# Kernel tuning notes

Hardware: AMD Instinct MI355X
Metric: run time of the kernel (lower is better)

The kernel has to match this reference:

```python
import jax, jax.numpy as jnp
import numpy as np

N = 50000       # nodes
E = 800000      # edges (avg degree 16)
NFEAT = 256
NHID = 32
NHEADS = 4
ALPHA = 0.2     # leaky relu slope


def setup_inputs() -> dict:
    key = jax.random.key(0)
    ks = jax.random.split(key, 7)
    x = jax.random.normal(ks[0], (N, NFEAT), dtype=jnp.float32)
    src = jax.random.randint(ks[1], (E,), 0, N, dtype=jnp.int32)
    dst = jax.random.randint(ks[2], (E,), 0, N, dtype=jnp.int32)
    Ws = jax.random.normal(ks[3], (NHEADS, NFEAT, NHID), dtype=jnp.float32) * 0.05
    As = jax.random.normal(ks[4], (NHEADS, 2 * NHID), dtype=jnp.float32) * 0.05
    Wo = jax.random.normal(ks[5], (NHID * NHEADS, NHID), dtype=jnp.float32) * 0.05
    Ao = jax.random.normal(ks[6], (2 * NHID,), dtype=jnp.float32) * 0.05
    return {"x": x, "src": src, "dst": dst, "Ws": Ws, "As": As, "Wo": Wo, "Ao": Ao}


def _gat_layer(h, src, dst, W, a, concat):
    # h: [N, F_in] -> project
    h = h @ W                          # [N, d]
    d = W.shape[1]
    hs = h[src]                        # [E, d] gather source feats
    hd = h[dst]                        # [E, d] gather neighbor feats
    # a . concat([hs, hd]) == hs @ a[:d] + hd @ a[d:]
    e = hs @ a[:d] + hd @ a[d:]        # [E]
    e = jnp.where(e > 0, e, ALPHA * e)  # leaky relu
    # segment softmax keyed on src
    m = jax.ops.segment_max(e, src, num_segments=N)    # [N]
    ex = jnp.exp(e - m[src])
    denom = jax.ops.segment_sum(ex, src, num_segments=N)  # [N]
    att = ex / denom[src]              # [E]
    # weighted neighbor aggregation (scatter-sum on src)
    h_prime = jax.ops.segment_sum(att[:, None] * hd, src, num_segments=N)  # [N, d]
    return jax.nn.elu(h_prime) if concat else h_prime


def reference(x, src, dst, Ws, As, Wo, Ao):
    heads = [_gat_layer(x, src, dst, Ws[i], As[i], concat=True) for i in range(NHEADS)]
    h = jnp.concatenate(heads, axis=1)                 # [N, nhid*nheads]
    out = jax.nn.elu(_gat_layer(h, src, dst, Wo, Ao, concat=False))  # [N, nhid]
    return out
```

## Files before the change

### kernel.cpp

```cpp
#include <hip/hip_runtime.h>
#include <hip/hip_fp16.h>
#include <math.h>

#define N_NODES 50000
#define N_EDGES 800000
#define NFEAT 256
#define NHID 32
#define NHEADS 4
#define ALPHA 0.2f
#define ELLCAP 64
#define ELLSH 6

typedef _Float16 half8_t __attribute__((ext_vector_type(8)));
typedef float f32x4 __attribute__((ext_vector_type(4)));

__device__ __forceinline__ float elu_f(float x) {
    return x > 0.0f ? x : (__expf(x) - 1.0f);
}

__device__ __forceinline__ float wexp(float x) {
    float l = x > 0.0f ? x : ALPHA * x;
    return __expf(l);
}

__device__ __forceinline__ float h2f_bits(unsigned wd, int sh) {
    ushort b = (ushort)(wd >> sh);
    return __half2float(*(__half*)&b);
}

__global__ void k_prep(const float* __restrict__ Ws, const float* __restrict__ Wo,
                       ushort* __restrict__ Wt1, ushort* __restrict__ Wt2) {
    int idx = blockIdx.x * 256 + threadIdx.x;
    if (idx < 128 * 256) {
        int c = idx >> 8;
        int k = idx & 255;
        __half hv = __float2half(Ws[(c >> 5) * (NFEAT * NHID) + k * NHID + (c & 31)]);
        Wt1[idx] = *(ushort*)&hv;
    } else if (idx < 128 * 256 + 32 * 128) {
        int j = idx - 128 * 256;
        int c = j >> 7;
        int k = j & 127;
        __half hv = __float2half(Wo[k * NHID + c]);
        Wt2[j] = *(ushort*)&hv;
    }
}

template <int K, int NTILES, bool AHALF, int NH>
__global__ __launch_bounds__(256) void k_gemm_mfma(const void* __restrict__ Ain,
                                                   const ushort* __restrict__ Wt,
                                                   const float* __restrict__ attn,
                                                   __half* __restrict__ C,
                                                   float* __restrict__ So,
                                                   float* __restrict__ Si,
                                                   int nrows) {
    constexpr int N = NTILES * 16;
    constexpr int BK = 32;
    constexpr int LDB = 40;

    __shared__ __align__(16) ushort Bs[N * LDB];

    int tid = threadIdx.x;
    int w = tid >> 6;
    int lane = tid & 63;
    int c = lane & 15;
    int quad = lane >> 4;
    int row0 = blockIdx.x * 64 + w * 16;
    int gm = row0 + c;
    if (gm >= nrows) gm = nrows - 1;

    f32x4 acc[NTILES];
#pragma unroll
    for (int nt = 0; nt < NTILES; nt++)
#pragma unroll
        for (int i = 0; i < 4; i++) acc[nt][i] = 0.0f;

    float a_so[NTILES], a_si[NTILES];
#pragma unroll
    for (int nt = 0; nt < NTILES; nt++) {
        int h = nt >> 1;
        a_so[nt] = attn[h * 64 + (nt & 1) * 16 + c];
        a_si[nt] = attn[h * 64 + 32 + (nt & 1) * 16 + c];
    }

    for (int k0 = 0; k0 < K; k0 += BK) {
        if (tid < N * 2) {
            int r = tid >> 1;
            int part = tid & 1;
            const uint4* gp = (const uint4*)(Wt + (size_t)r * K + k0 + part * 16);
            uint4 v0 = gp[0];
            uint4 v1 = gp[1];
            uint4* lp = (uint4*)&Bs[r * LDB + part * 16];
            lp[0] = v0;
            lp[1] = v1;
        }
        __syncthreads();

        half8_t ahi, alo;
        if constexpr (AHALF) {
            ahi = *(const half8_t*)((const ushort*)Ain + (size_t)gm * K + k0 + quad * 8);
        } else {
            const float* ap = (const float*)Ain + (size_t)gm * K + k0 + quad * 8;
            float4 x0 = *(const float4*)ap;
            float4 x1 = *(const float4*)(ap + 4);
            float xa[8] = {x0.x, x0.y, x0.z, x0.w, x1.x, x1.y, x1.z, x1.w};
#pragma unroll
            for (int j = 0; j < 8; j++) {
                _Float16 h = (_Float16)xa[j];
                ahi[j] = h;
                alo[j] = (_Float16)(xa[j] - (float)h);
            }
        }
#pragma unroll
        for (int nt = 0; nt < NTILES; nt++) {
            half8_t b = *(const half8_t*)&Bs[(nt * 16 + c) * LDB + quad * 8];
            acc[nt] = __builtin_amdgcn_mfma_f32_16x16x32_f16(ahi, b, acc[nt], 0, 0, 0);
            if constexpr (!AHALF)
                acc[nt] = __builtin_amdgcn_mfma_f32_16x16x32_f16(alo, b, acc[nt], 0, 0, 0);
        }
        __syncthreads();
    }

#pragma unroll
    for (int reg = 0; reg < 4; reg++) {
        int ro = row0 + quad * 4 + reg;
        bool ok = ro < nrows;
        if (ok) {
#pragma unroll
            for (int nt = 0; nt < NTILES; nt++)
                C[(size_t)ro * N + nt * 16 + c] = __float2half(acc[nt][reg]);
        }
#pragma unroll
        for (int h = 0; h < NH; h++) {
            float so = acc[2 * h][reg] * a_so[2 * h] + acc[2 * h + 1][reg] * a_so[2 * h + 1];
            float si = acc[2 * h][reg] * a_si[2 * h] + acc[2 * h + 1][reg] * a_si[2 * h + 1];
            so += __shfl_xor(so, 1); si += __shfl_xor(si, 1);
            so += __shfl_xor(so, 2); si += __shfl_xor(si, 2);
            so += __shfl_xor(so, 4); si += __shfl_xor(si, 4);
            so += __shfl_xor(so, 8); si += __shfl_xor(si, 8);
            if (c == 0 && ok) {
                So[(size_t)ro * NH + h] = so;
                Si[(size_t)ro * NH + h] = si;
            }
        }
    }
}

__global__ void k_fill(const int* __restrict__ src, const int* __restrict__ dst,
                       const float* __restrict__ S1o, const float* __restrict__ S1i,
                       int* __restrict__ deg, uint4* __restrict__ ell16,
                       int* __restrict__ eslot) {
    int e = blockIdx.x * 256 + threadIdx.x;
    if (e >= N_EDGES) return;
    int s = src[e];
    int v = dst[e];
    int slot = atomicAdd(&deg[s], 1);
    eslot[e] = slot;
    if (slot >= ELLCAP) return;
    float4 so = *(const float4*)(S1o + 4 * (size_t)s);
    float4 si = *(const float4*)(S1i + 4 * (size_t)v);
    __half2 w01 = __floats2half2_rn(wexp(so.x + si.x), wexp(so.y + si.y));
    __half2 w23 = __floats2half2_rn(wexp(so.z + si.z), wexp(so.w + si.w));
    uint4 q;
    q.x = (unsigned)v;
    q.y = *(unsigned*)&w01;
    q.z = *(unsigned*)&w23;
    q.w = 0;
    ell16[((size_t)s << ELLSH) + slot] = q;
}

__global__ __launch_bounds__(256) void k_aggw4(const int* __restrict__ deg,
                                               const uint4* __restrict__ ell16,
                                               const __half* __restrict__ H1h,
                                               __half* __restrict__ Hch) {
    int node = blockIdx.x * 4 + (threadIdx.x >> 6);
    if (node >= N_NODES) return;
    int lane = threadIdx.x & 63;
    int ha = lane >> 4;
    int sel = ha & 2;
    int sh = (ha & 1) * 16;
    int dg = deg[node];
    if (dg > ELLCAP) dg = ELLCAP;
    const uint4* lp = ell16 + ((size_t)node << ELLSH);
    const unsigned* Hp = (const unsigned*)H1h;
    float a0 = 0.0f, a1 = 0.0f, d = 0.0f;
    int j = 0;
    for (; j + 3 < dg; j += 4) {
        uint4 q0 = lp[j];
        uint4 q1 = lp[j + 1];
        uint4 q2 = lp[j + 2];
        uint4 q3 = lp[j + 3];
        unsigned u0 = Hp[((size_t)q0.x << 6) + lane];
        unsigned u1 = Hp[((size_t)q1.x << 6) + lane];
        unsigned u2 = Hp[((size_t)q2.x << 6) + lane];
        unsigned u3 = Hp[((size_t)q3.x << 6) + lane];
        float w0 = h2f_bits(sel ? q0.z : q0.y, sh);
        float w1 = h2f_bits(sel ? q1.z : q1.y, sh);
        float w2 = h2f_bits(sel ? q2.z : q2.y, sh);
        float w3 = h2f_bits(sel ? q3.z : q3.y, sh);
        float2 h0 = __half22float2(*(__half2*)&u0);
        float2 h1 = __half22float2(*(__half2*)&u1);
        float2 h2 = __half22float2(*(__half2*)&u2);
        float2 h3 = __half22float2(*(__half2*)&u3);
        a0 += w0 * h0.x; a1 += w0 * h0.y; d += w0;
        a0 += w1 * h1.x; a1 += w1 * h1.y; d += w1;
        a0 += w2 * h2.x; a1 += w2 * h2.y; d += w2;
        a0 += w3 * h3.x; a1 += w3 * h3.y; d += w3;
    }
    for (; j < dg; j++) {
        uint4 q0 = lp[j];
        unsigned u0 = Hp[((size_t)q0.x << 6) + lane];
        float w0 = h2f_bits(sel ? q0.z : q0.y, sh);
        float2 h0 = __half22float2(*(__half2*)&u0);
        a0 += w0 * h0.x; a1 += w0 * h0.y; d += w0;
    }
    float inv = d > 0.0f ? 1.0f / d : 0.0f;
    __half2 o = __floats2half2_rn(elu_f(a0 * inv), elu_f(a1 * inv));
    *(__half2*)(Hch + ((size_t)node << 7) + 2 * lane) = o;
}

__global__ void k_w2fill(const int* __restrict__ src, const int* __restrict__ dst,
                         const int* __restrict__ eslot,
                         const float* __restrict__ S2o, const float* __restrict__ S2i,
                         uint2* __restrict__ ew2) {
    int e = blockIdx.x * 256 + threadIdx.x;
    if (e >= N_EDGES) return;
    int s = src[e];
    int v = dst[e];
    int slot = eslot[e];
    if (slot >= ELLCAP) return;
    float w = wexp(S2o[s] + S2i[v]);
    uint2 q;
    q.x = (unsigned)v;
    q.y = __float_as_uint(w);
    ew2[((size_t)s << ELLSH) + slot] = q;
}

__global__ __launch_bounds__(256) void k_aggw2(const int* __restrict__ deg,
                                               const uint2* __restrict__ ew2,
                                               const __half* __restrict__ H2h,
                                               float* __restrict__ out) {
    int t = blockIdx.x * 256 + threadIdx.x;
    int node = t >> 4;
    if (node >= N_NODES) return;
    int l = t & 15;
    int dg = deg[node];
    if (dg > ELLCAP) dg = ELLCAP;
    const uint2* lp = ew2 + ((size_t)node << ELLSH);
    const unsigned* Hp = (const unsigned*)H2h;
    float a0 = 0.0f, a1 = 0.0f, d = 0.0f;
    int j = 0;
    for (; j + 3 < dg; j += 4) {
        uint2 q0 = lp[j];
        uint2 q1 = lp[j + 1];
        uint2 q2 = lp[j + 2];
        uint2 q3 = lp[j + 3];
        unsigned u0 = Hp[((size_t)q0.x << 4) + l];
        unsigned u1 = Hp[((size_t)q1.x << 4) + l];
        unsigned u2 = Hp[((size_t)q2.x << 4) + l];
        unsigned u3 = Hp[((size_t)q3.x << 4) + l];
        float w0 = __uint_as_float(q0.y);
        float w1 = __uint_as_float(q1.y);
        float w2 = __uint_as_float(q2.y);
        float w3 = __uint_as_float(q3.y);
        float2 h0 = __half22float2(*(__half2*)&u0);
        float2 h1 = __half22float2(*(__half2*)&u1);
        float2 h2 = __half22float2(*(__half2*)&u2);
        float2 h3 = __half22float2(*(__half2*)&u3);
        a0 += w0 * h0.x; a1 += w0 * h0.y; d += w0;
        a0 += w1 * h1.x; a1 += w1 * h1.y; d += w1;
        a0 += w2 * h2.x; a1 += w2 * h2.y; d += w2;
        a0 += w3 * h3.x; a1 += w3 * h3.y; d += w3;
    }
    for (; j < dg; j++) {
        uint2 q0 = lp[j];
        unsigned u0 = Hp[((size_t)q0.x << 4) + l];
        float w0 = __uint_as_float(q0.y);
        float2 h0 = __half22float2(*(__half2*)&u0);
        a0 += w0 * h0.x; a1 += w0 * h0.y; d += w0;
    }
    float inv = d > 0.0f ? 1.0f / d : 0.0f;
    float2 o = make_float2(elu_f(a0 * inv), elu_f(a1 * inv));
    *(float2*)(out + ((size_t)node << 5) + 2 * l) = o;
}

extern "C" void kernel_launch(void* const* d_in, const int* in_sizes, int n_in,
                              void* d_out, int out_size, void* d_ws, size_t ws_size,
                              hipStream_t stream) {
    const float* x = (const float*)d_in[0];
    const int* src = (const int*)d_in[1];
    const int* dst = (const int*)d_in[2];
    const float* Ws = (const float*)d_in[3];
    const float* As = (const float*)d_in[4];
    const float* Wo = (const float*)d_in[5];
    const float* Ao = (const float*)d_in[6];
    float* out = (float*)d_out;

    char* p = (char*)d_ws;
    auto alloc = [&](size_t bytes) -> void* {
        void* r = (void*)p;
        p += (bytes + 255) & ~(size_t)255;
        return r;
    };
    ushort* Wt1 = (ushort*)alloc((size_t)128 * 256 * 2);
    ushort* Wt2 = (ushort*)alloc((size_t)32 * 128 * 2);
    __half* H1h = (__half*)alloc((size_t)N_NODES * 128 * 2);
    __half* Hch = (__half*)alloc((size_t)N_NODES * 128 * 2);
    uint2* ew2 = (uint2*)H1h;
    __half* H2h = (__half*)alloc((size_t)N_NODES * 32 * 2);
    float* S1o = (float*)alloc((size_t)N_NODES * 4 * 4);
    float* S1i = (float*)alloc((size_t)N_NODES * 4 * 4);
    float* S2o = (float*)alloc((size_t)N_NODES * 4);
    float* S2i = (float*)alloc((size_t)N_NODES * 4);
    int* deg   = (int*)alloc((size_t)N_NODES * 4);
    int* eslot = (int*)alloc((size_t)N_EDGES * 4);
    uint4* ell16 = (uint4*)alloc((size_t)N_NODES * ELLCAP * 16);

    const int EDGE_BLKS = (N_EDGES + 255) / 256;
    const int GEMM_BLKS = (N_NODES + 63) / 64;

    hipMemsetAsync(deg, 0, (size_t)N_NODES * 4, stream);

    k_prep<<<(128 * 256 + 32 * 128 + 255) / 256, 256, 0, stream>>>(Ws, Wo, Wt1, Wt2);

    k_gemm_mfma<256, 8, false, 4><<<GEMM_BLKS, 256, 0, stream>>>(
        x, Wt1, As, H1h, S1o, S1i, N_NODES);

    k_fill<<<EDGE_BLKS, 256, 0, stream>>>(src, dst, S1o, S1i, deg, ell16, eslot);

    k_aggw4<<<(N_NODES + 3) / 4, 256, 0, stream>>>(deg, ell16, H1h, Hch);

    k_gemm_mfma<128, 2, true, 1><<<GEMM_BLKS, 256, 0, stream>>>(
        Hch, Wt2, Ao, H2h, S2o, S2i, N_NODES);

    k_w2fill<<<EDGE_BLKS, 256, 0, stream>>>(src, dst, eslot, S2o, S2i, ew2);

    k_aggw2<<<(N_NODES * 16 + 255) / 256, 256, 0, stream>>>(deg, ew2, H2h, out);
}
```

Before: 243.7 us.

## Fuse GEMM1 with ELL build and compute edge weights inside aggregation

Layer-1 GEMM and the edge-to-ELL fill now run as two block ranges of one kernel, so they can overlap. The ELL stores only 16-bit neighbor ids. Attention weights are computed per node inside both aggregation kernels and staged in shared memory, which removes the separate weight-fill kernels and the eslot array. Zeroing deg is folded into the prep kernel in place of a memset. This cuts launches and ELL write/read traffic, at the cost of extra exp work and a block barrier in the aggregation kernels, and it relies on node ids fitting in 16 bits.

```diff
diff --git a/kernel.cpp b/kernel.cpp
--- a/kernel.cpp
+++ b/kernel.cpp
@@ -11,6 +11,9 @@
 #define ELLCAP 64
 #define ELLSH 6
 
+#define GEMM1_BLKS ((N_NODES + 63) / 64)
+#define FILL_BLKS ((N_EDGES + 255) / 256)
+
 typedef _Float16 half8_t __attribute__((ext_vector_type(8)));
 typedef float f32x4 __attribute__((ext_vector_type(4)));
 
@@ -29,7 +32,8 @@
 }
 
 __global__ void k_prep(const float* __restrict__ Ws, const float* __restrict__ Wo,
-                       ushort* __restrict__ Wt1, ushort* __restrict__ Wt2) {
+                       ushort* __restrict__ Wt1, ushort* __restrict__ Wt2,
+                       int* __restrict__ deg) {
     int idx = blockIdx.x * 256 + threadIdx.x;
     if (idx < 128 * 256) {
         int c = idx >> 8;
@@ -43,16 +47,18 @@
         __half hv = __float2half(Wo[k * NHID + c]);
         Wt2[j] = *(ushort*)&hv;
     }
+    int z = idx - (128 * 256 + 32 * 128);
+    if (z >= 0 && z < N_NODES) deg[z] = 0;
 }
 
 template <int K, int NTILES, bool AHALF, int NH>
-__global__ __launch_bounds__(256) void k_gemm_mfma(const void* __restrict__ Ain,
-                                                   const ushort* __restrict__ Wt,
-                                                   const float* __restrict__ attn,
-                                                   __half* __restrict__ C,
-                                                   float* __restrict__ So,
-                                                   float* __restrict__ Si,
-                                                   int nrows) {
+__device__ __forceinline__ void gemm_body(const void* __restrict__ Ain,
+                                          const ushort* __restrict__ Wt,
+                                          const float* __restrict__ attn,
+                                          __half* __restrict__ C,
+                                          float* __restrict__ So,
+                                          float* __restrict__ Si,
+                                          int nrows, int bid) {
     constexpr int N = NTILES * 16;
     constexpr int BK = 32;
     constexpr int LDB = 40;
@@ -64,7 +70,7 @@
     int lane = tid & 63;
     int c = lane & 15;
     int quad = lane >> 4;
-    int row0 = blockIdx.x * 64 + w * 16;
+    int row0 = bid * 64 + w * 16;
     int gm = row0 + c;
     if (gm >= nrows) gm = nrows - 1;
 
@@ -145,50 +151,74 @@
     }
 }
 
-__global__ void k_fill(const int* __restrict__ src, const int* __restrict__ dst,
-                       const float* __restrict__ S1o, const float* __restrict__ S1i,
-                       int* __restrict__ deg, uint4* __restrict__ ell16,
-                       int* __restrict__ eslot) {
-    int e = blockIdx.x * 256 + threadIdx.x;
-    if (e >= N_EDGES) return;
-    int s = src[e];
-    int v = dst[e];
-    int slot = atomicAdd(&deg[s], 1);
-    eslot[e] = slot;
-    if (slot >= ELLCAP) return;
-    float4 so = *(const float4*)(S1o + 4 * (size_t)s);
-    float4 si = *(const float4*)(S1i + 4 * (size_t)v);
-    __half2 w01 = __floats2half2_rn(wexp(so.x + si.x), wexp(so.y + si.y));
-    __half2 w23 = __floats2half2_rn(wexp(so.z + si.z), wexp(so.w + si.w));
-    uint4 q;
-    q.x = (unsigned)v;
-    q.y = *(unsigned*)&w01;
-    q.z = *(unsigned*)&w23;
-    q.w = 0;
-    ell16[((size_t)s << ELLSH) + slot] = q;
+__global__ __launch_bounds__(256) void k_g1fill(const float* __restrict__ x,
+                                                const ushort* __restrict__ Wt1,
+                                                const float* __restrict__ attn,
+                                                __half* __restrict__ H1h,
+                                                float* __restrict__ S1o,
+                                                float* __restrict__ S1i,
+                                                const int* __restrict__ src,
+                                                const int* __restrict__ dst,
+                                                int* __restrict__ deg,
+                                                ushort* __restrict__ ell2) {
+    if (blockIdx.x < GEMM1_BLKS) {
+        gemm_body<256, 8, false, 4>(x, Wt1, attn, H1h, S1o, S1i, N_NODES, blockIdx.x);
+    } else {
+        int e = (blockIdx.x - GEMM1_BLKS) * 256 + threadIdx.x;
+        if (e < N_EDGES) {
+            int s = src[e];
+            int v = dst[e];
+            int slot = atomicAdd(&deg[s], 1);
+            if (slot < ELLCAP) ell2[((size_t)s << ELLSH) + slot] = (ushort)v;
+        }
+    }
+}
+
+__global__ __launch_bounds__(256) void k_gemm2(const __half* __restrict__ Hch,
+                                               const ushort* __restrict__ Wt2,
+                                               const float* __restrict__ attn,
+                                               __half* __restrict__ H2h,
+                                               float* __restrict__ S2o,
+                                               float* __restrict__ S2i) {
+    gemm_body<128, 2, true, 1>(Hch, Wt2, attn, H2h, S2o, S2i, N_NODES, blockIdx.x);
 }
 
 __global__ __launch_bounds__(256) void k_aggw4(const int* __restrict__ deg,
-                                               const uint4* __restrict__ ell16,
+                                               const ushort* __restrict__ ell2,
+                                               const float* __restrict__ S1o,
+                                               const float* __restrict__ S1i,
                                                const __half* __restrict__ H1h,
                                                __half* __restrict__ Hch) {
-    int node = blockIdx.x * 4 + (threadIdx.x >> 6);
-    if (node >= N_NODES) return;
+    __shared__ uint4 ew[4][ELLCAP];
+    int wv = threadIdx.x >> 6;
+    int node = blockIdx.x * 4 + wv;
     int lane = threadIdx.x & 63;
-    int ha = lane >> 4;
-    int sel = ha & 2;
-    int sh = (ha & 1) * 16;
     int dg = deg[node];
     if (dg > ELLCAP) dg = ELLCAP;
-    const uint4* lp = ell16 + ((size_t)node << ELLSH);
+    if (lane < dg) {
+        int v = ell2[((size_t)node << ELLSH) + lane];
+        float4 so = *(const float4*)(S1o + 4 * (size_t)node);
+        float4 si = *(const float4*)(S1i + 4 * (size_t)v);
+        __half2 w01 = __floats2half2_rn(wexp(so.x + si.x), wexp(so.y + si.y));
+        __half2 w23 = __floats2half2_rn(wexp(so.z + si.z), wexp(so.w + si.w));
+        uint4 q;
+        q.x = (unsigned)v;
+        q.y = *(unsigned*)&w01;
+        q.z = *(unsigned*)&w23;
+        q.w = 0;
+        ew[wv][lane] = q;
+    }
+    __syncthreads();
+    int sel = (lane >> 4) & 2;
+    int sh = ((lane >> 4) & 1) * 16;
     const unsigned* Hp = (const unsigned*)H1h;
     float a0 = 0.0f, a1 = 0.0f, d = 0.0f;
     int j = 0;
     for (; j + 3 < dg; j += 4) {
-        uint4 q0 = lp[j];
-        uint4 q1 = lp[j + 1];
-        uint4 q2 = lp[j + 2];
-        uint4 q3 = lp[j + 3];
+        uint4 q0 = ew[wv][j];
+        uint4 q1 = ew[wv][j + 1];
+        uint4 q2 = ew[wv][j + 2];
+        uint4 q3 = ew[wv][j + 3];
         unsigned u0 = Hp[((size_t)q0.x << 6) + lane];
         unsigned u1 = Hp[((size_t)q1.x << 6) + lane];
         unsigned u2 = Hp[((size_t)q2.x << 6) + lane];
@@ -207,7 +237,7 @@
         a0 += w3 * h3.x; a1 += w3 * h3.y; d += w3;
     }
     for (; j < dg; j++) {
-        uint4 q0 = lp[j];
+        uint4 q0 = ew[wv][j];
         unsigned u0 = Hp[((size_t)q0.x << 6) + lane];
         float w0 = h2f_bits(sel ? q0.z : q0.y, sh);
         float2 h0 = __half22float2(*(__half2*)&u0);
@@ -218,42 +248,41 @@
     *(__half2*)(Hch + ((size_t)node << 7) + 2 * lane) = o;
 }
 
-__global__ void k_w2fill(const int* __restrict__ src, const int* __restrict__ dst,
-                         const int* __restrict__ eslot,
-                         const float* __restrict__ S2o, const float* __restrict__ S2i,
-                         uint2* __restrict__ ew2) {
-    int e = blockIdx.x * 256 + threadIdx.x;
-    if (e >= N_EDGES) return;
-    int s = src[e];
-    int v = dst[e];
-    int slot = eslot[e];
-    if (slot >= ELLCAP) return;
-    float w = wexp(S2o[s] + S2i[v]);
-    uint2 q;
-    q.x = (unsigned)v;
-    q.y = __float_as_uint(w);
-    ew2[((size_t)s << ELLSH) + slot] = q;
-}
-
 __global__ __launch_bounds__(256) void k_aggw2(const int* __restrict__ deg,
-                                               const uint2* __restrict__ ew2,
+                                               const ushort* __restrict__ ell2,
+                                               const float* __restrict__ S2o,
+                                               const float* __restrict__ S2i,
                                                const __half* __restrict__ H2h,
                                                float* __restrict__ out) {
+    __shared__ uint2 ew[16][ELLCAP];
     int t = blockIdx.x * 256 + threadIdx.x;
     int node = t >> 4;
-    if (node >= N_NODES) return;
+    int ng = (threadIdx.x >> 4);
     int l = t & 15;
     int dg = deg[node];
     if (dg > ELLCAP) dg = ELLCAP;
-    const uint2* lp = ew2 + ((size_t)node << ELLSH);
+    float so = S2o[node];
+#pragma unroll
+    for (int k = 0; k < 4; k++) {
+        int j = l + k * 16;
+        if (j < dg) {
+            int v = ell2[((size_t)node << ELLSH) + j];
+            float w = wexp(so + S2i[v]);
+            uint2 q;
+            q.x = (unsigned)v;
+            q.y = __float_as_uint(w);
+            ew[ng][j] = q;
+        }
+    }
+    __syncthreads();
     const unsigned* Hp = (const unsigned*)H2h;
     float a0 = 0.0f, a1 = 0.0f, d = 0.0f;
     int j = 0;
     for (; j + 3 < dg; j += 4) {
-        uint2 q0 = lp[j];
-        uint2 q1 = lp[j + 1];
-        uint2 q2 = lp[j + 2];
-        uint2 q3 = lp[j + 3];
+        uint2 q0 = ew[ng][j];
+        uint2 q1 = ew[ng][j + 1];
+        uint2 q2 = ew[ng][j + 2];
+        uint2 q3 = ew[ng][j + 3];
         unsigned u0 = Hp[((size_t)q0.x << 4) + l];
         unsigned u1 = Hp[((size_t)q1.x << 4) + l];
         unsigned u2 = Hp[((size_t)q2.x << 4) + l];
@@ -272,7 +301,7 @@
         a0 += w3 * h3.x; a1 += w3 * h3.y; d += w3;
     }
     for (; j < dg; j++) {
-        uint2 q0 = lp[j];
+        uint2 q0 = ew[ng][j];
         unsigned u0 = Hp[((size_t)q0.x << 4) + l];
         float w0 = __uint_as_float(q0.y);
         float2 h0 = __half22float2(*(__half2*)&u0);
@@ -305,34 +334,23 @@
     ushort* Wt2 = (ushort*)alloc((size_t)32 * 128 * 2);
     __half* H1h = (__half*)alloc((size_t)N_NODES * 128 * 2);
     __half* Hch = (__half*)alloc((size_t)N_NODES * 128 * 2);
-    uint2* ew2 = (uint2*)H1h;
     __half* H2h = (__half*)alloc((size_t)N_NODES * 32 * 2);
     float* S1o = (float*)alloc((size_t)N_NODES * 4 * 4);
     float* S1i = (float*)alloc((size_t)N_NODES * 4 * 4);
     float* S2o = (float*)alloc((size_t)N_NODES * 4);
     float* S2i = (float*)alloc((size_t)N_NODES * 4);
     int* deg   = (int*)alloc((size_t)N_NODES * 4);
-    int* eslot = (int*)alloc((size_t)N_EDGES * 4);
-    uint4* ell16 = (uint4*)alloc((size_t)N_NODES * ELLCAP * 16);
-
-    const int EDGE_BLKS = (N_EDGES + 255) / 256;
-    const int GEMM_BLKS = (N_NODES + 63) / 64;
-
-    hipMemsetAsync(deg, 0, (size_t)N_NODES * 4, stream);
-
-    k_prep<<<(128 * 256 + 32 * 128 + 255) / 256, 256, 0, stream>>>(Ws, Wo, Wt1, Wt2);
-
-    k_gemm_mfma<256, 8, false, 4><<<GEMM_BLKS, 256, 0, stream>>>(
-        x, Wt1, As, H1h, S1o, S1i, N_NODES);
-
-    k_fill<<<EDGE_BLKS, 256, 0, stream>>>(src, dst, S1o, S1i, deg, ell16, eslot);
-
-    k_aggw4<<<(N_NODES + 3) / 4, 256, 0, stream>>>(deg, ell16, H1h, Hch);
-
-    k_gemm_mfma<128, 2, true, 1><<<GEMM_BLKS, 256, 0, stream>>>(
-        Hch, Wt2, Ao, H2h, S2o, S2i, N_NODES);
-
-    k_w2fill<<<EDGE_BLKS, 256, 0, stream>>>(src, dst, eslot, S2o, S2i, ew2);
-
-    k_aggw2<<<(N_NODES * 16 + 255) / 256, 256, 0, stream>>>(deg, ew2, H2h, out);
-}
+    ushort* ell2 = (ushort*)alloc((size_t)N_NODES * ELLCAP * 2);
+
+    const int PREP_THREADS = 128 * 256 + 32 * 128 + N_NODES;
+    k_prep<<<(PREP_THREADS + 255) / 256, 256, 0, stream>>>(Ws, Wo, Wt1, Wt2, deg);
+
+    k_g1fill<<<GEMM1_BLKS + FILL_BLKS, 256, 0, stream>>>(
+        x, Wt1, As, H1h, S1o, S1i, src, dst, deg, ell2);
+
+    k_aggw4<<<(N_NODES + 3) / 4, 256, 0, stream>>>(deg, ell2, S1o, S1i, H1h, Hch);
+
+    k_gemm2<<<(N_NODES + 63) / 64, 256, 0, stream>>>(Hch, Wt2, Ao, H2h, S2o, S2i);
+
+    k_aggw2<<<(N_NODES * 16 + 255) / 256, 256, 0, stream>>>(deg, ell2, S2o, S2i, H2h, out);
+}
```

Measured after the change: 202.9 us. 16.8% less time.
